# Optimization experiments

Measured on AMD Instinct MI355X. Metric: run time of the kernel, lower is better.

## Reference

```python
import jax, jax.numpy as jnp
import numpy as np

B, N, C = 4, 4096, 32
S = 4096  # samples == N (square DFT matrix)


def setup_inputs() -> dict:
    key = jax.random.key(0)
    k1, k2 = jax.random.split(key)
    x = jax.random.normal(k1, (B, N, C), dtype=jnp.float32)
    t = jax.random.uniform(k2, (B, N), dtype=jnp.float32)  # sample times in [0,1]
    # learnable freqs initialized exactly as in the module: linspace(0,1,samples)
    freqs = jnp.linspace(0.0, 1.0, S).astype(jnp.float32)
    return {"x": x, "t": t, "freqs": freqs}


def reference(x, t, freqs):
    n = x.shape[1]
    # exponent_rows = -2*pi*i * (freqs*(n-1)) / n  -> purely imaginary, keep the real phase
    rows = (-2.0 * jnp.pi / n) * (freqs * (n - 1))          # [S]
    cols = t * (n - 1)                                       # [B, N]
    phase = rows[None, :, None] * cols[:, None, :]           # [B, S, N]
    fourier = jnp.exp(1j * phase.astype(jnp.complex64)) * (1.0 / np.sqrt(n)).astype(np.float32)
    z = jnp.einsum('bsn,bnc->bsc', fourier, x.astype(jnp.complex64))  # [B, S, C] complex
    # remove_zerocomp: zero first and last output rows
    z = z.at[:, 0].set(0).at[:, -1].set(0)
    # real=True -> magnitude as float32
    return jnp.abs(z).astype(jnp.float32)
```

## Files before the change

kernel.cpp:

```cpp
#include <hip/hip_runtime.h>
#include <hip/hip_fp16.h>
#include <math.h>

#define B_ 4
#define N_ 4096
#define C_ 32
#define S_ 4096
#define KW 512
#define NSTEP 16

typedef float f32x4 __attribute__((ext_vector_type(4)));
typedef _Float16 f16x8 __attribute__((ext_vector_type(8)));
typedef __fp16 fp16x2 __attribute__((ext_vector_type(2)));
typedef unsigned int uint_t;
typedef unsigned short ushort_t;

#define XTH_OFF 0
#define PSI_OFF (B_ * C_ * N_ * 2)
#define WS_NEED (PSI_OFF + B_ * N_ * 4)

__device__ __forceinline__ uint_t pkrtz(float a, float b) {
    union { fp16x2 h; uint_t w; } u;
    u.h = __builtin_amdgcn_cvt_pkrtz(a, b);
    return u.w;
}

__device__ __forceinline__ void sincos_ref(float p, float& sn, float& cs) {
    const double INV2PI_D = 0.15915494309189535;
    const float HI = (float)INV2PI_D;
    const float LO = (float)(INV2PI_D - (double)HI);
    float hi = p * HI;
    float e  = fmaf(p, HI, -hi);
    e = fmaf(p, LO, e);
    float k = rintf(hi);
    float r = (hi - k) + e;
    sn = __builtin_amdgcn_sinf(r);
    cs = __builtin_amdgcn_cosf(r);
}

__global__ __launch_bounds__(256)
void fudft_prep(const float* __restrict__ x, const float* __restrict__ t,
                ushort_t* __restrict__ xTh, float* __restrict__ psi)
{
    __shared__ ushort_t lds[64][40];
    const int tid = threadIdx.x;
    const int n0 = blockIdx.x * 64;
    const int b  = blockIdx.y;

    const float* src = x + ((size_t)b * N_ + n0) * C_;
    const int nl = tid >> 2, c0 = (tid & 3) * 8;
    const float4 v0 = *(const float4*)(src + (size_t)nl * C_ + c0);
    const float4 v1 = *(const float4*)(src + (size_t)nl * C_ + c0 + 4);
    const float vv[8] = {v0.x, v0.y, v0.z, v0.w, v1.x, v1.y, v1.z, v1.w};
    union { ushort_t u[8]; int4 i; } hp;
#pragma unroll
    for (int j = 0; j < 8; ++j) hp.u[j] = __half_as_ushort(__float2half_rn(vv[j]));
    *(int4*)&lds[nl][c0] = hp.i;

    if (tid < 64) psi[b * N_ + n0 + tid] = t[b * N_ + n0 + tid] * (float)(N_ - 1);
    __syncthreads();

    const int c = tid >> 3, oct = tid & 7;
    union { ushort_t u[8]; int4 i; } o;
#pragma unroll
    for (int j = 0; j < 8; ++j) o.u[j] = lds[oct * 8 + j][c];
    *(int4*)(xTh + ((size_t)(b * C_ + c)) * N_ + n0 + oct * 8) = o.i;
}

#define MFMA16(A, Bv, Acc) __builtin_amdgcn_mfma_f32_16x16x32_f16(A, Bv, Acc, 0, 0, 0)

__global__ __launch_bounds__(512, 4)
void fudft_mfma(const float* __restrict__ freqs,
                const ushort_t* __restrict__ xTh,
                const float* __restrict__ psi,
                float* __restrict__ out)
{
    __shared__ float red[14336];

    const int tid = threadIdx.x;
    const int wk = tid >> 6;
    const int lane = tid & 63;
    const int q = lane >> 4, r = lane & 15;
    const int b = blockIdx.y;
    const int sb = blockIdx.x * 32;

    const float rr0 = -(freqs[sb + r]      * (float)(N_ - 1)) * 0.000244140625f;
    const float rr1 = -(freqs[sb + 16 + r] * (float)(N_ - 1)) * 0.000244140625f;

    const float* pp = psi + b * N_ + wk * KW + q * 8;
    const ushort_t* xb0 = xTh + ((size_t)(b * C_ + r)) * N_ + wk * KW + q * 8;
    const ushort_t* xb1 = xb0 + 16 * N_;

    f32x4 aRe0a = {0,0,0,0}, aIm0a = {0,0,0,0}, aRe0b = {0,0,0,0}, aIm0b = {0,0,0,0};
    f32x4 aRe1a = {0,0,0,0}, aIm1a = {0,0,0,0}, aRe1b = {0,0,0,0}, aIm1b = {0,0,0,0};

#pragma unroll 4
    for (int s = 0; s < NSTEP; ++s) {
        const float4 p0 = *(const float4*)(pp + s * 32);
        const float4 p1 = *(const float4*)(pp + s * 32 + 4);
        union { int4 i; f16x8 v; } b0, b1;
        b0.i = *(const int4*)(xb0 + s * 32);
        b1.i = *(const int4*)(xb1 + s * 32);

        const float ph[8] = {p0.x, p0.y, p0.z, p0.w, p1.x, p1.y, p1.z, p1.w};
        float c0v[8], s0v[8], c1v[8], s1v[8];
#pragma unroll
        for (int j = 0; j < 8; ++j) {
            float rv0 = rr0 * ph[j]; rv0 -= floorf(rv0);
            s0v[j] = __builtin_amdgcn_sinf(rv0);
            c0v[j] = __builtin_amdgcn_cosf(rv0);
            float rv1 = rr1 * ph[j]; rv1 -= floorf(rv1);
            s1v[j] = __builtin_amdgcn_sinf(rv1);
            c1v[j] = __builtin_amdgcn_cosf(rv1);
        }
        union { uint_t w[4]; f16x8 v; } fC0, fS0, fC1, fS1;
#pragma unroll
        for (int j = 0; j < 4; ++j) {
            fC0.w[j] = pkrtz(c0v[2*j], c0v[2*j+1]);
            fS0.w[j] = pkrtz(s0v[2*j], s0v[2*j+1]);
            fC1.w[j] = pkrtz(c1v[2*j], c1v[2*j+1]);
            fS1.w[j] = pkrtz(s1v[2*j], s1v[2*j+1]);
        }
        aRe0a = MFMA16(fC0.v, b0.v, aRe0a);  aRe0b = MFMA16(fC0.v, b1.v, aRe0b);
        aIm0a = MFMA16(fS0.v, b0.v, aIm0a);  aIm0b = MFMA16(fS0.v, b1.v, aIm0b);
        aRe1a = MFMA16(fC1.v, b0.v, aRe1a);  aRe1b = MFMA16(fC1.v, b1.v, aRe1b);
        aIm1a = MFMA16(fS1.v, b0.v, aIm1a);  aIm1b = MFMA16(fS1.v, b1.v, aIm1b);
    }

    if (wk > 0) {
        float* rb = red + (size_t)(wk - 1) * 8 * 256 + lane * 4;
        *(f32x4*)(rb + 0*256) = aRe0a;  *(f32x4*)(rb + 1*256) = aIm0a;
        *(f32x4*)(rb + 2*256) = aRe0b;  *(f32x4*)(rb + 3*256) = aIm0b;
        *(f32x4*)(rb + 4*256) = aRe1a;  *(f32x4*)(rb + 5*256) = aIm1a;
        *(f32x4*)(rb + 6*256) = aRe1b;  *(f32x4*)(rb + 7*256) = aIm1b;
    }
    __syncthreads();
    if (wk == 0) {
#pragma unroll
        for (int sl = 0; sl < 7; ++sl) {
            const float* rb = red + (size_t)sl * 8 * 256 + lane * 4;
            aRe0a += *(const f32x4*)(rb + 0*256);  aIm0a += *(const f32x4*)(rb + 1*256);
            aRe0b += *(const f32x4*)(rb + 2*256);  aIm0b += *(const f32x4*)(rb + 3*256);
            aRe1a += *(const f32x4*)(rb + 4*256);  aIm1a += *(const f32x4*)(rb + 5*256);
            aRe1b += *(const f32x4*)(rb + 6*256);  aIm1b += *(const f32x4*)(rb + 7*256);
        }
        float* po = out + ((size_t)b * S_ + sb) * C_;
#pragma unroll
        for (int reg = 0; reg < 4; ++reg) {
            const int m0 = q * 4 + reg, m1 = 16 + q * 4 + reg;
            const bool z0 = (sb + m0 == 0) || (sb + m0 == S_ - 1);
            const bool z1 = (sb + m1 == 0) || (sb + m1 == S_ - 1);
            float v;
            v = sqrtf(fmaf(aRe0a[reg], aRe0a[reg], aIm0a[reg]*aIm0a[reg])) * 0.015625f;
            po[(size_t)m0 * C_ + r]      = z0 ? 0.f : v;
            v = sqrtf(fmaf(aRe0b[reg], aRe0b[reg], aIm0b[reg]*aIm0b[reg])) * 0.015625f;
            po[(size_t)m0 * C_ + 16 + r] = z0 ? 0.f : v;
            v = sqrtf(fmaf(aRe1a[reg], aRe1a[reg], aIm1a[reg]*aIm1a[reg])) * 0.015625f;
            po[(size_t)m1 * C_ + r]      = z1 ? 0.f : v;
            v = sqrtf(fmaf(aRe1b[reg], aRe1b[reg], aIm1b[reg]*aIm1b[reg])) * 0.015625f;
            po[(size_t)m1 * C_ + 16 + r] = z1 ? 0.f : v;
        }
    }
}

__global__ __launch_bounds__(256)
void fudft_naive(const float* __restrict__ x, const float* __restrict__ t,
                 const float* __restrict__ freqs, float* __restrict__ out)
{
    const int s = blockIdx.x * 256 + threadIdx.x;
    const int b = blockIdx.y;
    const float row = (freqs[s] * (float)(N_ - 1)) * (float)(-2.0 * M_PI / (double)N_);
    float aR[C_], aI[C_];
#pragma unroll
    for (int c = 0; c < C_; ++c) { aR[c] = 0.f; aI[c] = 0.f; }
    for (int n = 0; n < N_; ++n) {
        const float col = t[b * N_ + n] * (float)(N_ - 1);
        float sn, cs; sincos_ref(row * col, sn, cs);
        const float* xr = x + ((size_t)b * N_ + n) * C_;
#pragma unroll
        for (int c = 0; c < C_; ++c) {
            aR[c] = fmaf(cs, xr[c], aR[c]);
            aI[c] = fmaf(sn, xr[c], aI[c]);
        }
    }
    float* dst = out + ((size_t)b * S_ + s) * C_;
    const bool zero = (s == 0) || (s == S_ - 1);
#pragma unroll
    for (int c = 0; c < C_; ++c) {
        const float m = sqrtf(fmaf(aR[c], aR[c], aI[c] * aI[c])) * 0.015625f;
        dst[c] = zero ? 0.f : m;
    }
}

extern "C" void kernel_launch(void* const* d_in, const int* in_sizes, int n_in,
                              void* d_out, int out_size, void* d_ws, size_t ws_size,
                              hipStream_t stream) {
    const float* x = (const float*)d_in[0];
    const float* t = (const float*)d_in[1];
    const float* f = (const float*)d_in[2];
    float* out = (float*)d_out;

    if (ws_size >= (size_t)WS_NEED) {
        char* ws = (char*)d_ws;
        ushort_t* xTh = (ushort_t*)(ws + XTH_OFF);
        float*    psi = (float*)(ws + PSI_OFF);

        dim3 gprep(N_ / 64, B_);
        fudft_prep<<<gprep, 256, 0, stream>>>(x, t, xTh, psi);
        dim3 grid(S_ / 32, B_);
        fudft_mfma<<<grid, 512, 0, stream>>>(f, xTh, psi, out);
    } else {
        dim3 grid(S_ / 256, B_);
        fudft_naive<<<grid, 256, 0, stream>>>(x, t, f, out);
    }
}
```

Baseline: 81.91 us.

## Stage psi in LDS via async loads, prefetch x, tree-reduce partials

Each block now copies its batch's psi row into shared memory with global_load_lds, and every wave reads phases from LDS instead of global memory. The x fragments are software-pipelined by one step so the next load overlaps the current MFMAs. The cross-wave reduction becomes a log-tree in a smaller 32KB LDS buffer, which lets the occupancy hint rise to 6 blocks, and floor-subtract is replaced with the hardware fract instruction. In exchange the reduction needs more barriers, and the larger occupancy target may pressure registers.

```diff
diff --git a/kernel.cpp b/kernel.cpp
--- a/kernel.cpp
+++ b/kernel.cpp
@@ -14,6 +14,9 @@
 typedef __fp16 fp16x2 __attribute__((ext_vector_type(2)));
 typedef unsigned int uint_t;
 typedef unsigned short ushort_t;
+
+#define AS1(p) ((const __attribute__((address_space(1))) void*)(p))
+#define AS3(p) ((__attribute__((address_space(3))) void*)(p))
 
 #define XTH_OFF 0
 #define PSI_OFF (B_ * C_ * N_ * 2)
@@ -69,47 +72,62 @@
 
 #define MFMA16(A, Bv, Acc) __builtin_amdgcn_mfma_f32_16x16x32_f16(A, Bv, Acc, 0, 0, 0)
 
-__global__ __launch_bounds__(512, 4)
+__global__ __launch_bounds__(512, 6)
 void fudft_mfma(const float* __restrict__ freqs,
                 const ushort_t* __restrict__ xTh,
                 const float* __restrict__ psi,
                 float* __restrict__ out)
 {
-    __shared__ float red[14336];
+    __shared__ __align__(16) float sred[8192];
 
     const int tid = threadIdx.x;
     const int wk = tid >> 6;
+    const int wid = wk;
     const int lane = tid & 63;
     const int q = lane >> 4, r = lane & 15;
     const int b = blockIdx.y;
     const int sb = blockIdx.x * 32;
 
+    {
+        const float* pg = psi + (size_t)b * N_;
+        __builtin_amdgcn_global_load_lds(AS1(pg + tid * 4),        AS3(sred + wid * 256),        16, 0, 0);
+        __builtin_amdgcn_global_load_lds(AS1(pg + 2048 + tid * 4), AS3(sred + 2048 + wid * 256), 16, 0, 0);
+    }
+
     const float rr0 = -(freqs[sb + r]      * (float)(N_ - 1)) * 0.000244140625f;
     const float rr1 = -(freqs[sb + 16 + r] * (float)(N_ - 1)) * 0.000244140625f;
 
-    const float* pp = psi + b * N_ + wk * KW + q * 8;
     const ushort_t* xb0 = xTh + ((size_t)(b * C_ + r)) * N_ + wk * KW + q * 8;
     const ushort_t* xb1 = xb0 + 16 * N_;
+    const float* pl = sred + wk * KW + q * 8;
 
     f32x4 aRe0a = {0,0,0,0}, aIm0a = {0,0,0,0}, aRe0b = {0,0,0,0}, aIm0b = {0,0,0,0};
     f32x4 aRe1a = {0,0,0,0}, aIm1a = {0,0,0,0}, aRe1b = {0,0,0,0}, aIm1b = {0,0,0,0};
 
-#pragma unroll 4
+    union { int4 i; f16x8 v; } b0c, b1c, b0n, b1n;
+    b0c.i = *(const int4*)(xb0);
+    b1c.i = *(const int4*)(xb1);
+
+    asm volatile("s_waitcnt vmcnt(0)" ::: "memory");
+    __syncthreads();
+
+#pragma unroll 2
     for (int s = 0; s < NSTEP; ++s) {
-        const float4 p0 = *(const float4*)(pp + s * 32);
-        const float4 p1 = *(const float4*)(pp + s * 32 + 4);
-        union { int4 i; f16x8 v; } b0, b1;
-        b0.i = *(const int4*)(xb0 + s * 32);
-        b1.i = *(const int4*)(xb1 + s * 32);
+        if (s + 1 < NSTEP) {
+            b0n.i = *(const int4*)(xb0 + (s + 1) * 32);
+            b1n.i = *(const int4*)(xb1 + (s + 1) * 32);
+        }
+        const float4 p0 = *(const float4*)(pl + s * 32);
+        const float4 p1 = *(const float4*)(pl + s * 32 + 4);
 
         const float ph[8] = {p0.x, p0.y, p0.z, p0.w, p1.x, p1.y, p1.z, p1.w};
         float c0v[8], s0v[8], c1v[8], s1v[8];
 #pragma unroll
         for (int j = 0; j < 8; ++j) {
-            float rv0 = rr0 * ph[j]; rv0 -= floorf(rv0);
+            float rv0 = __builtin_amdgcn_fractf(rr0 * ph[j]);
             s0v[j] = __builtin_amdgcn_sinf(rv0);
             c0v[j] = __builtin_amdgcn_cosf(rv0);
-            float rv1 = rr1 * ph[j]; rv1 -= floorf(rv1);
+            float rv1 = __builtin_amdgcn_fractf(rr1 * ph[j]);
             s1v[j] = __builtin_amdgcn_sinf(rv1);
             c1v[j] = __builtin_amdgcn_cosf(rv1);
         }
@@ -121,29 +139,41 @@
             fC1.w[j] = pkrtz(c1v[2*j], c1v[2*j+1]);
             fS1.w[j] = pkrtz(s1v[2*j], s1v[2*j+1]);
         }
-        aRe0a = MFMA16(fC0.v, b0.v, aRe0a);  aRe0b = MFMA16(fC0.v, b1.v, aRe0b);
-        aIm0a = MFMA16(fS0.v, b0.v, aIm0a);  aIm0b = MFMA16(fS0.v, b1.v, aIm0b);
-        aRe1a = MFMA16(fC1.v, b0.v, aRe1a);  aRe1b = MFMA16(fC1.v, b1.v, aRe1b);
-        aIm1a = MFMA16(fS1.v, b0.v, aIm1a);  aIm1b = MFMA16(fS1.v, b1.v, aIm1b);
-    }
-
-    if (wk > 0) {
-        float* rb = red + (size_t)(wk - 1) * 8 * 256 + lane * 4;
+        aRe0a = MFMA16(fC0.v, b0c.v, aRe0a);  aRe0b = MFMA16(fC0.v, b1c.v, aRe0b);
+        aIm0a = MFMA16(fS0.v, b0c.v, aIm0a);  aIm0b = MFMA16(fS0.v, b1c.v, aIm0b);
+        aRe1a = MFMA16(fC1.v, b0c.v, aRe1a);  aRe1b = MFMA16(fC1.v, b1c.v, aRe1b);
+        aIm1a = MFMA16(fS1.v, b0c.v, aIm1a);  aIm1b = MFMA16(fS1.v, b1c.v, aIm1b);
+        b0c = b0n; b1c = b1n;
+    }
+
+    auto store_slot = [&](int slot) {
+        float* rb = sred + slot * 2048 + lane * 4;
         *(f32x4*)(rb + 0*256) = aRe0a;  *(f32x4*)(rb + 1*256) = aIm0a;
         *(f32x4*)(rb + 2*256) = aRe0b;  *(f32x4*)(rb + 3*256) = aIm0b;
         *(f32x4*)(rb + 4*256) = aRe1a;  *(f32x4*)(rb + 5*256) = aIm1a;
         *(f32x4*)(rb + 6*256) = aRe1b;  *(f32x4*)(rb + 7*256) = aIm1b;
-    }
+    };
+    auto add_slot = [&](int slot) {
+        const float* rb = sred + slot * 2048 + lane * 4;
+        aRe0a += *(const f32x4*)(rb + 0*256);  aIm0a += *(const f32x4*)(rb + 1*256);
+        aRe0b += *(const f32x4*)(rb + 2*256);  aIm0b += *(const f32x4*)(rb + 3*256);
+        aRe1a += *(const f32x4*)(rb + 4*256);  aIm1a += *(const f32x4*)(rb + 5*256);
+        aRe1b += *(const f32x4*)(rb + 6*256);  aIm1b += *(const f32x4*)(rb + 7*256);
+    };
+
+    __syncthreads();
+    if (wk >= 4) store_slot(wk - 4);
+    __syncthreads();
+    if (wk < 4) add_slot(wk);
+    __syncthreads();
+    if (wk == 2 || wk == 3) store_slot(wk - 2);
+    __syncthreads();
+    if (wk < 2) add_slot(wk);
+    __syncthreads();
+    if (wk == 1) store_slot(0);
     __syncthreads();
     if (wk == 0) {
-#pragma unroll
-        for (int sl = 0; sl < 7; ++sl) {
-            const float* rb = red + (size_t)sl * 8 * 256 + lane * 4;
-            aRe0a += *(const f32x4*)(rb + 0*256);  aIm0a += *(const f32x4*)(rb + 1*256);
-            aRe0b += *(const f32x4*)(rb + 2*256);  aIm0b += *(const f32x4*)(rb + 3*256);
-            aRe1a += *(const f32x4*)(rb + 4*256);  aIm1a += *(const f32x4*)(rb + 5*256);
-            aRe1b += *(const f32x4*)(rb + 6*256);  aIm1b += *(const f32x4*)(rb + 7*256);
-        }
+        add_slot(0);
         float* po = out + ((size_t)b * S_ + sb) * C_;
 #pragma unroll
         for (int reg = 0; reg < 4; ++reg) {
```

New measurement: 82.76 us. Within noise of the previous version (+1.0%).
